# Kernel tuning notes

Hardware: AMD Instinct MI355X
Metric: run time of the kernel (lower is better)

Reference implementation:

```python
import jax, jax.numpy as jnp
import numpy as np

NUM_HEADS = 16
SRC_FACTS = 4


def setup_inputs() -> dict:
    key = jax.random.key(0)
    k1, k2, k3, k4, k5 = jax.random.split(key, 5)
    B, S, H, Dh = 16, 512, NUM_HEADS, 64  # B = batch(4) * src_facts(4)
    D = H * Dh  # d_model = 1024
    pre_q = jax.random.normal(k1, (B, S, H, Dh), dtype=jnp.float32)
    pre_v = jax.random.normal(k2, (B, S, H, Dh), dtype=jnp.float32)
    pre_k = jax.random.normal(k3, (B, S, H, Dh), dtype=jnp.float32)
    attn_mask = jax.random.randint(k4, (B, S, S), 0, 2).astype(jnp.int32)
    output_weights = jax.random.normal(k5, (D, D), dtype=jnp.float32) / np.float32(np.sqrt(D))
    return {
        "pre_q": pre_q,
        "pre_v": pre_v,
        "pre_k": pre_k,
        "attn_mask": attn_mask,
        "output_weights": output_weights,
        "out_seq_len": 512,
        "d_model": 1024,
    }


def reference(pre_q, pre_v, pre_k, attn_mask, output_weights, out_seq_len, d_model):
    B, Sq, H, Dh = pre_q.shape
    # Original: K.sqrt(cast(d_model) // num_heads) -> sqrt(head_dim)
    scale = jnp.sqrt(jnp.float32(float(d_model) // H))
    mask = attn_mask.astype(jnp.float32)[:, None]  # (B, 1, q, k) broadcast over heads
    # scores: (B, H, q, k)
    scores = jnp.einsum("bqhd,bkhd->bhqk", pre_q, pre_k) / scale
    # multiplicative pre-mask + additive -1e9 on masked slots
    scores = scores * mask + (1.0 - mask) * jnp.float32(-1e9)
    # softmax then multiplicative post-mask
    attn = jax.nn.softmax(scores, axis=-1) * mask
    heads = jnp.einsum("bhqk,bkhd->bqhd", attn, pre_v)  # (B, q, H, Dh)
    out = heads.reshape(B, Sq, H * Dh) @ output_weights  # (B, q, d_model)
    return out.reshape(-1, SRC_FACTS, out_seq_len, d_model)
```

## Files before the change

kernel.cpp:

```cpp
#include <hip/hip_runtime.h>
#include <hip/hip_bf16.h>


typedef __bf16 bf16;
typedef bf16 bf16x8 __attribute__((ext_vector_type(8)));
typedef bf16 bf16x4 __attribute__((ext_vector_type(4)));
typedef float floatx4 __attribute__((ext_vector_type(4)));
typedef float floatx16 __attribute__((ext_vector_type(16)));
typedef unsigned short ushort8 __attribute__((ext_vector_type(8)));
typedef unsigned long long u64;

#define MFMA32(A, B, C)    __builtin_amdgcn_mfma_f32_16x16x32_bf16((A), (B), (C), 0, 0, 0)
#define MFMA32x32(A, B, C) __builtin_amdgcn_mfma_f32_32x32x16_bf16((A), (B), (C), 0, 0, 0)

namespace {
constexpr int S   = 512;
constexpr int H   = 16;
constexpr int Dh  = 64;
constexpr int D   = 1024;
constexpr int LDT = 72;
constexpr size_t QN = (size_t)16 * S * H * Dh;
constexpr size_t WN = (size_t)D * D;
}

__device__ __forceinline__ float fexp2(float x) {
#if defined(__HIP_DEVICE_COMPILE__) && __has_builtin(__builtin_amdgcn_exp2f)
    return __builtin_amdgcn_exp2f(x);
#else
    return exp2f(x);
#endif
}

__device__ __forceinline__ int sbfe1(unsigned bits, int bit) {
    return ((int)(bits << (31 - bit))) >> 31;
}

__device__ __forceinline__ void gload16(const bf16* g, bf16* ldsbase, int lane) {
#if __has_builtin(__builtin_amdgcn_global_load_lds)
    __builtin_amdgcn_global_load_lds(
        (__attribute__((address_space(1))) void*)(g),
        (__attribute__((address_space(3))) void*)(ldsbase), 16, 0, 0);
#else
    *(ushort8*)(ldsbase + lane * 8) = *(const ushort8*)g;
#endif
}

__global__ __launch_bounds__(256)
void prep_kernel(const float* __restrict__ Kf, const float* __restrict__ Vf,
                 const float* __restrict__ Wf, const int* __restrict__ Mg,
                 bf16* __restrict__ Kc, bf16* __restrict__ Vt,
                 bf16* __restrict__ Wt, u64* __restrict__ MB)
{
    __shared__ bf16 Ts[64 * LDT];
    const int blk = blockIdx.x, tid = threadIdx.x;

    if (blk < 1024) {
        const int c0 = blk * 1024 + tid;
        floatx4 f[4][2];
#pragma unroll
        for (int k = 0; k < 4; ++k) {
            const float* fs = Kf + (size_t)(c0 + k * 256) * 8;
            f[k][0] = *(const floatx4*)fs;
            f[k][1] = *(const floatx4*)(fs + 4);
        }
#pragma unroll
        for (int k = 0; k < 4; ++k) {
            bf16x8 v;
#pragma unroll
            for (int j = 0; j < 4; ++j) {
                v[j]     = (bf16)f[k][0][j];
                v[j + 4] = (bf16)f[k][1][j];
            }
            *(bf16x8*)(Kc + (size_t)(c0 + k * 256) * 8) = v;
        }
    } else if (blk < 3072) {
        const int bk2 = blk - 1024;
        const int bh  = bk2 >> 3, st = bk2 & 7;
        const int b   = bh >> 4, h = bh & 15;
        const int r   = tid >> 2, c = (tid & 3) * 16;
        const float* src = Vf + ((size_t)((b * S + st * 64 + r) * H + h)) * Dh + c;
#pragma unroll
        for (int i = 0; i < 16; ++i)
            Ts[(c + i) * LDT + (r ^ ((c + i) & 48))] = (bf16)src[i];
        __syncthreads();
        bf16* dst = Vt + ((size_t)bh * 64 + r) * S + st * 64 + c;
        const int rb = r * LDT + (c ^ (r & 48));
        *(ushort8*)dst       = *(const ushort8*)&Ts[rb];
        *(ushort8*)(dst + 8) = *(const ushort8*)&Ts[rb + 8];
    } else if (blk < 3328) {
        const int bk2 = blk - 3072;
        const int nb  = bk2 & 15, kb = bk2 >> 4;
        const int r   = tid >> 2, c = (tid & 3) * 16;
        const float* src = Wf + (size_t)(kb * 64 + r) * D + nb * 64 + c;
#pragma unroll
        for (int i = 0; i < 16; ++i)
            Ts[(c + i) * LDT + (r ^ ((c + i) & 48))] = (bf16)src[i];
        __syncthreads();
        bf16* dst = Wt + (size_t)(nb * 64 + r) * D + kb * 64 + c;
        const int rb = r * LDT + (c ^ (r & 48));
        *(ushort8*)dst       = *(const ushort8*)&Ts[rb];
        *(ushort8*)(dst + 8) = *(const ushort8*)&Ts[rb + 8];
    } else {
        const int bk2  = blk - 3328;
        const int lane = tid & 63;
        const int wv   = tid >> 6;
        const int u0   = bk2 * 16 + wv * 4;
        int mv[4][4];
#pragma unroll
        for (int u = 0; u < 4; ++u) {
            const int idx4 = u0 + u;
            const int row = idx4 >> 1, hf = idx4 & 1;
#pragma unroll
            for (int r = 0; r < 4; ++r)
                mv[u][r] = Mg[(size_t)row * 512 + hf * 256 + r * 64 + lane];
        }
#pragma unroll
        for (int u = 0; u < 4; ++u) {
            const int idx4 = u0 + u;
            const int row = idx4 >> 1, hf = idx4 & 1;
#pragma unroll
            for (int r = 0; r < 4; ++r) {
                u64 bm = __ballot(mv[u][r] != 0);
                if (lane == 0) MB[(size_t)row * 8 + hf * 4 + r] = bm;
            }
        }
    }
}

__global__ __launch_bounds__(256, 4)
void attn_kernel(const float* __restrict__ Qg, const bf16* __restrict__ Kc,
                 const bf16* __restrict__ Vtg, const u64* __restrict__ MB,
                 bf16* __restrict__ heads)
{
    __shared__ bf16 Ks[64 * LDT];
    __shared__ bf16 Vt[64 * LDT];

    const int tid  = threadIdx.x;
    const int lane = tid & 63;
    const int wave = tid >> 6;
    const int l31  = lane & 31;
    const int half = lane >> 5;

    const int blk = blockIdx.x;
    const int h   = blk & 15;
    const int qt  = (blk >> 4) & 3;
    const int b   = blk >> 6;
    const int qw  = qt * 128 + wave * 32;

    constexpr float QSCL = 0.125f * 1.44269504088896340736f;
    bf16x8 aq[4];
    {
        const float* qb = Qg + ((size_t)((b * S + qw + l31) * H + h)) * Dh + half * 8;
#pragma unroll
        for (int ds = 0; ds < 4; ++ds) {
            floatx4 f0 = *(const floatx4*)(qb + ds * 16);
            floatx4 f1 = *(const floatx4*)(qb + ds * 16 + 4);
#pragma unroll
            for (int j = 0; j < 4; ++j) {
                aq[ds][j]     = (bf16)(f0[j] * QSCL);
                aq[ds][j + 4] = (bf16)(f1[j] * QSCL);
            }
        }
    }

    float rsum = 0.f;
    floatx16 O[2];
#pragma unroll
    for (int dt = 0; dt < 2; ++dt)
#pragma unroll
        for (int i = 0; i < 16; ++i) O[dt][i] = 0.f;

    const u64* mbrow = MB + ((size_t)b * S + qw + l31) * 8;
    const bf16* vplane = Vtg + (size_t)(b * 16 + h) * 64 * S;

    const int sr = tid >> 2, sc_ = (tid & 3) * 16;
    const int kperm = (sr & 0x33) | ((sr & 4) << 1) | ((sr & 8) >> 1);

    for (int kt = 0; kt < 8; ++kt) {
        const int kb = kt * 64;
        const bf16* ksrc = Kc + ((size_t)((b * S + kb + kperm) * H + h)) * Dh + sc_;
        const bf16* vsrc = vplane + (size_t)sr * S + kb + sc_;
        ushort8 k0 = *(const ushort8*)ksrc;
        ushort8 k1 = *(const ushort8*)(ksrc + 8);
        ushort8 v0 = *(const ushort8*)vsrc;
        ushort8 v1 = *(const ushort8*)(vsrc + 8);
        u64 m64 = mbrow[kt];

        __syncthreads();
        *(ushort8*)&Ks[sr * LDT + sc_]     = k0;
        *(ushort8*)&Ks[sr * LDT + sc_ + 8] = k1;
        *(ushort8*)&Vt[sr * LDT + sc_]     = v0;
        *(ushort8*)&Vt[sr * LDT + sc_ + 8] = v1;
        __syncthreads();

        bf16x8 pB[4];
#pragma unroll
        for (int t = 0; t < 2; ++t) {
            floatx16 acc;
#pragma unroll
            for (int i = 0; i < 16; ++i) acc[i] = 0.f;
#pragma unroll
            for (int ds = 0; ds < 4; ++ds) {
                bf16x8 ak = *(const bf16x8*)&Ks[(t * 32 + l31) * LDT + ds * 16 + half * 8];
                acc = MFMA32x32(ak, aq[ds], acc);
            }
            const unsigned w = (unsigned)(m64 >> (t * 32 + half * 8));
#pragma unroll
            for (int r = 0; r < 16; ++r) {
                float e = fexp2(acc[r]);
                int sx = sbfe1(w, (r >> 3) * 16 + (r & 7));
                float p = __uint_as_float(__float_as_uint(e) & (unsigned)sx);
                rsum += p;
                pB[t * 2 + (r >> 3)][r & 7] = (bf16)p;
            }
        }

#pragma unroll
        for (int dt = 0; dt < 2; ++dt)
#pragma unroll
            for (int s_ = 0; s_ < 4; ++s_) {
                bf16x8 av = *(const bf16x8*)&Vt[(dt * 32 + l31) * LDT + s_ * 16 + half * 8];
                O[dt] = MFMA32x32(av, pB[s_], O[dt]);
            }
    }

    rsum += __shfl_xor(rsum, 32, 64);
    const float inv = (rsum > 0.f) ? (1.f / rsum) : 0.f;

    bf16* hrow = heads + ((size_t)((b * S + qw + l31) * H + h)) * Dh;
#pragma unroll
    for (int dt = 0; dt < 2; ++dt) {
#pragma unroll
        for (int g = 0; g < 4; ++g) {
            bf16x4 h4;
#pragma unroll
            for (int j = 0; j < 4; ++j) h4[j] = (bf16)(O[dt][g * 4 + j] * inv);
            *(bf16x4*)&hrow[dt * 32 + g * 8 + half * 4] = h4;
        }
    }
}

__global__ __launch_bounds__(256)
void proj_kernel(const bf16* __restrict__ A, const bf16* __restrict__ Wt,
                 float* __restrict__ out)
{
    __shared__ bf16 As[128 * 32];
    __shared__ bf16 Ws[128 * 32];

    const int tid  = threadIdx.x;
    const int lane = tid & 63;
    const int wave = tid >> 6;
    const int l15  = lane & 15;
    const int quad = lane >> 4;

    const int nb = blockIdx.x & 7;
    const int mb = blockIdx.x >> 3;
    const int mbase = mb * 128, nbase = nb * 128;
    const int wm = (wave & 1) * 64, wn = (wave >> 1) * 64;

    const int ch0  = wave * 2;
    const int srow = lane >> 2;
    const int scol = (lane & 3) * 8;

    floatx4 O[4][4];
#pragma unroll
    for (int mt = 0; mt < 4; ++mt)
#pragma unroll
        for (int nt = 0; nt < 4; ++nt) O[mt][nt] = floatx4{0.f, 0.f, 0.f, 0.f};

    for (int kt = 0; kt < 32; ++kt) {
        const int kb = kt * 32;
        if (kt) __syncthreads();

        gload16(A  + (size_t)(mbase + ch0 * 16      + srow) * D + kb + scol, As + ch0 * 512,       lane);
        gload16(A  + (size_t)(mbase + (ch0 + 1) * 16 + srow) * D + kb + scol, As + (ch0 + 1) * 512, lane);
        gload16(Wt + (size_t)(nbase + ch0 * 16      + srow) * D + kb + scol, Ws + ch0 * 512,       lane);
        gload16(Wt + (size_t)(nbase + (ch0 + 1) * 16 + srow) * D + kb + scol, Ws + (ch0 + 1) * 512, lane);

        __syncthreads();

        bf16x8 fa[4];
#pragma unroll
        for (int mt = 0; mt < 4; ++mt)
            fa[mt] = *(const bf16x8*)&As[(wm + mt * 16 + l15) * 32 + quad * 8];
#pragma unroll
        for (int nt = 0; nt < 4; ++nt) {
            bf16x8 fb = *(const bf16x8*)&Ws[(wn + nt * 16 + l15) * 32 + quad * 8];
#pragma unroll
            for (int mt = 0; mt < 4; ++mt)
                O[mt][nt] = MFMA32(fa[mt], fb, O[mt][nt]);
        }
    }

#pragma unroll
    for (int mt = 0; mt < 4; ++mt) {
#pragma unroll
        for (int nt = 0; nt < 4; ++nt) {
#pragma unroll
            for (int reg = 0; reg < 4; ++reg) {
                const int m = mbase + wm + mt * 16 + quad * 4 + reg;
                const int n = nbase + wn + nt * 16 + l15;
                out[(size_t)m * D + n] = O[mt][nt][reg];
            }
        }
    }
}

extern "C" void kernel_launch(void* const* d_in, const int* in_sizes, int n_in,
                              void* d_out, int out_size, void* d_ws, size_t ws_size,
                              hipStream_t stream)
{
    const float* pre_q = (const float*)d_in[0];
    const float* pre_v = (const float*)d_in[1];
    const float* pre_k = (const float*)d_in[2];
    const int*   mask  = (const int*)d_in[3];
    const float* Wg    = (const float*)d_in[4];
    float* out = (float*)d_out;

    bf16* Kc    = (bf16*)d_ws;
    bf16* Vt    = Kc + QN;
    bf16* Wt    = Vt + QN;
    bf16* heads = Wt + WN;
    u64*  MB    = (u64*)(heads + QN);

    prep_kernel<<<4352, 256, 0, stream>>>(pre_k, pre_v, Wg, mask, Kc, Vt, Wt, MB);
    attn_kernel<<<1024, 256, 0, stream>>>(pre_q, Kc, Vt, MB, heads);
    proj_kernel<<<512, 256, 0, stream>>>(heads, Wt, out);
}
```

Baseline: 209.4 us.

## Load K and V tiles directly from global memory, dropping LDS staging

Removes the shared-memory staging of K and V tiles and the two block-wide barriers per key tile. Each wave now loads its MFMA operands straight from global memory (through L1/L2), with the permuted key row computed per lane. This removes LDS write traffic and synchronisation. In exchange, each of the four waves loads the same K/V data separately, which raises global/cache traffic and exposes load latency with no explicit prefetch.

```diff
diff --git a/kernel.cpp b/kernel.cpp
--- a/kernel.cpp
+++ b/kernel.cpp
@@ -132,9 +132,6 @@
                  const bf16* __restrict__ Vtg, const u64* __restrict__ MB,
                  bf16* __restrict__ heads)
 {
-    __shared__ bf16 Ks[64 * LDT];
-    __shared__ bf16 Vt[64 * LDT];
-
     const int tid  = threadIdx.x;
     const int lane = tid & 63;
     const int wave = tid >> 6;
@@ -171,37 +168,25 @@
         for (int i = 0; i < 16; ++i) O[dt][i] = 0.f;
 
     const u64* mbrow = MB + ((size_t)b * S + qw + l31) * 8;
-    const bf16* vplane = Vtg + (size_t)(b * 16 + h) * 64 * S;
-
-    const int sr = tid >> 2, sc_ = (tid & 3) * 16;
-    const int kperm = (sr & 0x33) | ((sr & 4) << 1) | ((sr & 8) >> 1);
+
+    const int sl = (l31 & 0x13) | ((l31 & 4) << 1) | ((l31 & 8) >> 1);
+    const bf16* klane = Kc + ((size_t)((b * S + sl) * H + h)) * Dh + half * 8;
+    const bf16* vlane = Vtg + (size_t)(b * 16 + h) * 64 * S + (size_t)l31 * S + half * 8;
 
     for (int kt = 0; kt < 8; ++kt) {
         const int kb = kt * 64;
-        const bf16* ksrc = Kc + ((size_t)((b * S + kb + kperm) * H + h)) * Dh + sc_;
-        const bf16* vsrc = vplane + (size_t)sr * S + kb + sc_;
-        ushort8 k0 = *(const ushort8*)ksrc;
-        ushort8 k1 = *(const ushort8*)(ksrc + 8);
-        ushort8 v0 = *(const ushort8*)vsrc;
-        ushort8 v1 = *(const ushort8*)(vsrc + 8);
-        u64 m64 = mbrow[kt];
-
-        __syncthreads();
-        *(ushort8*)&Ks[sr * LDT + sc_]     = k0;
-        *(ushort8*)&Ks[sr * LDT + sc_ + 8] = k1;
-        *(ushort8*)&Vt[sr * LDT + sc_]     = v0;
-        *(ushort8*)&Vt[sr * LDT + sc_ + 8] = v1;
-        __syncthreads();
+        const u64 m64 = mbrow[kt];
 
         bf16x8 pB[4];
 #pragma unroll
         for (int t = 0; t < 2; ++t) {
+            const bf16* kp = klane + (size_t)(kb + t * 32) * (H * Dh);
             floatx16 acc;
 #pragma unroll
             for (int i = 0; i < 16; ++i) acc[i] = 0.f;
 #pragma unroll
             for (int ds = 0; ds < 4; ++ds) {
-                bf16x8 ak = *(const bf16x8*)&Ks[(t * 32 + l31) * LDT + ds * 16 + half * 8];
+                bf16x8 ak = *(const bf16x8*)(kp + ds * 16);
                 acc = MFMA32x32(ak, aq[ds], acc);
             }
             const unsigned w = (unsigned)(m64 >> (t * 32 + half * 8));
@@ -216,12 +201,14 @@
         }
 
 #pragma unroll
-        for (int dt = 0; dt < 2; ++dt)
+        for (int dt = 0; dt < 2; ++dt) {
+            const bf16* vp = vlane + (size_t)dt * 32 * S + kb;
 #pragma unroll
             for (int s_ = 0; s_ < 4; ++s_) {
-                bf16x8 av = *(const bf16x8*)&Vt[(dt * 32 + l31) * LDT + s_ * 16 + half * 8];
+                bf16x8 av = *(const bf16x8*)(vp + s_ * 16);
                 O[dt] = MFMA32x32(av, pB[s_], O[dt]);
             }
+        }
     }
 
     rsum += __shfl_xor(rsum, 32, 64);
```

After: 250.5 us. +19.6%, slower.

## Double projection K-tile to 64 with XOR-swizzled LDS and vectorize transpose loads

Applied to the files above, without the earlier changes.

The projection GEMM now stages 64-wide K slices per iteration instead of 32, which halves the number of barrier and load rounds. It uses an XOR swizzle on the 16-byte chunk index so that the wider LDS rows avoid bank conflicts on fragment reads. The V and W transpose-cast paths now read their 16 floats as four float4 vector loads instead of scalar loads. The cost is double the LDS per block, which may lower occupancy.

```diff
diff --git a/kernel.cpp b/kernel.cpp
--- a/kernel.cpp
+++ b/kernel.cpp
@@ -79,9 +79,17 @@
         const int b   = bh >> 4, h = bh & 15;
         const int r   = tid >> 2, c = (tid & 3) * 16;
         const float* src = Vf + ((size_t)((b * S + st * 64 + r) * H + h)) * Dh + c;
-#pragma unroll
-        for (int i = 0; i < 16; ++i)
-            Ts[(c + i) * LDT + (r ^ ((c + i) & 48))] = (bf16)src[i];
+        floatx4 f0 = *(const floatx4*)src;
+        floatx4 f1 = *(const floatx4*)(src + 4);
+        floatx4 f2 = *(const floatx4*)(src + 8);
+        floatx4 f3 = *(const floatx4*)(src + 12);
+#pragma unroll
+        for (int i = 0; i < 4; ++i) {
+            Ts[(c + i)      * LDT + (r ^ ((c + i)      & 48))] = (bf16)f0[i];
+            Ts[(c + 4 + i)  * LDT + (r ^ ((c + 4 + i)  & 48))] = (bf16)f1[i];
+            Ts[(c + 8 + i)  * LDT + (r ^ ((c + 8 + i)  & 48))] = (bf16)f2[i];
+            Ts[(c + 12 + i) * LDT + (r ^ ((c + 12 + i) & 48))] = (bf16)f3[i];
+        }
         __syncthreads();
         bf16* dst = Vt + ((size_t)bh * 64 + r) * S + st * 64 + c;
         const int rb = r * LDT + (c ^ (r & 48));
@@ -92,9 +100,17 @@
         const int nb  = bk2 & 15, kb = bk2 >> 4;
         const int r   = tid >> 2, c = (tid & 3) * 16;
         const float* src = Wf + (size_t)(kb * 64 + r) * D + nb * 64 + c;
-#pragma unroll
-        for (int i = 0; i < 16; ++i)
-            Ts[(c + i) * LDT + (r ^ ((c + i) & 48))] = (bf16)src[i];
+        floatx4 f0 = *(const floatx4*)src;
+        floatx4 f1 = *(const floatx4*)(src + 4);
+        floatx4 f2 = *(const floatx4*)(src + 8);
+        floatx4 f3 = *(const floatx4*)(src + 12);
+#pragma unroll
+        for (int i = 0; i < 4; ++i) {
+            Ts[(c + i)      * LDT + (r ^ ((c + i)      & 48))] = (bf16)f0[i];
+            Ts[(c + 4 + i)  * LDT + (r ^ ((c + 4 + i)  & 48))] = (bf16)f1[i];
+            Ts[(c + 8 + i)  * LDT + (r ^ ((c + 8 + i)  & 48))] = (bf16)f2[i];
+            Ts[(c + 12 + i) * LDT + (r ^ ((c + 12 + i) & 48))] = (bf16)f3[i];
+        }
         __syncthreads();
         bf16* dst = Wt + (size_t)(nb * 64 + r) * D + kb * 64 + c;
         const int rb = r * LDT + (c ^ (r & 48));
@@ -244,8 +260,8 @@
 void proj_kernel(const bf16* __restrict__ A, const bf16* __restrict__ Wt,
                  float* __restrict__ out)
 {
-    __shared__ bf16 As[128 * 32];
-    __shared__ bf16 Ws[128 * 32];
+    __shared__ bf16 As[128 * 64];
+    __shared__ bf16 Ws[128 * 64];
 
     const int tid  = threadIdx.x;
     const int lane = tid & 63;
@@ -258,9 +274,8 @@
     const int mbase = mb * 128, nbase = nb * 128;
     const int wm = (wave & 1) * 64, wn = (wave >> 1) * 64;
 
-    const int ch0  = wave * 2;
-    const int srow = lane >> 2;
-    const int scol = (lane & 3) * 8;
+    const int srow = lane >> 3;
+    const int scsw = ((lane & 7) ^ (lane >> 3)) * 8;
 
     floatx4 O[4][4];
 #pragma unroll
@@ -268,27 +283,40 @@
 #pragma unroll
         for (int nt = 0; nt < 4; ++nt) O[mt][nt] = floatx4{0.f, 0.f, 0.f, 0.f};
 
-    for (int kt = 0; kt < 32; ++kt) {
-        const int kb = kt * 32;
+    for (int kt = 0; kt < 16; ++kt) {
+        const int kb = kt * 64;
         if (kt) __syncthreads();
 
-        gload16(A  + (size_t)(mbase + ch0 * 16      + srow) * D + kb + scol, As + ch0 * 512,       lane);
-        gload16(A  + (size_t)(mbase + (ch0 + 1) * 16 + srow) * D + kb + scol, As + (ch0 + 1) * 512, lane);
-        gload16(Wt + (size_t)(nbase + ch0 * 16      + srow) * D + kb + scol, Ws + ch0 * 512,       lane);
-        gload16(Wt + (size_t)(nbase + (ch0 + 1) * 16 + srow) * D + kb + scol, Ws + (ch0 + 1) * 512, lane);
-
-        __syncthreads();
-
-        bf16x8 fa[4];
-#pragma unroll
-        for (int mt = 0; mt < 4; ++mt)
-            fa[mt] = *(const bf16x8*)&As[(wm + mt * 16 + l15) * 32 + quad * 8];
+#pragma unroll
+        for (int j = 0; j < 4; ++j) {
+            const int rowbase = j * 32 + wave * 8;
+            gload16(A  + (size_t)(mbase + rowbase + srow) * D + kb + scsw,
+                    As + rowbase * 64, lane);
+            gload16(Wt + (size_t)(nbase + rowbase + srow) * D + kb + scsw,
+                    Ws + rowbase * 64, lane);
+        }
+
+        __syncthreads();
+
+        bf16x8 fa[4][2];
+#pragma unroll
+        for (int mt = 0; mt < 4; ++mt) {
+            const int row = wm + mt * 16 + l15;
+            const int sw  = row & 7;
+            fa[mt][0] = *(const bf16x8*)&As[row * 64 + ((quad ^ sw) * 8)];
+            fa[mt][1] = *(const bf16x8*)&As[row * 64 + (((quad + 4) ^ sw) * 8)];
+        }
 #pragma unroll
         for (int nt = 0; nt < 4; ++nt) {
-            bf16x8 fb = *(const bf16x8*)&Ws[(wn + nt * 16 + l15) * 32 + quad * 8];
-#pragma unroll
-            for (int mt = 0; mt < 4; ++mt)
-                O[mt][nt] = MFMA32(fa[mt], fb, O[mt][nt]);
+            const int row = wn + nt * 16 + l15;
+            const int sw  = row & 7;
+            bf16x8 fb0 = *(const bf16x8*)&Ws[row * 64 + ((quad ^ sw) * 8)];
+            bf16x8 fb1 = *(const bf16x8*)&Ws[row * 64 + (((quad + 4) ^ sw) * 8)];
+#pragma unroll
+            for (int mt = 0; mt < 4; ++mt) {
+                O[mt][nt] = MFMA32(fa[mt][0], fb0, O[mt][nt]);
+                O[mt][nt] = MFMA32(fa[mt][1], fb1, O[mt][nt]);
+            }
         }
     }
 
```

Result: no change. 206.4 us (-1.4%).
